# Optimization experiments

Hardware: AMD Instinct MI355X
Metric: run time of the kernel (lower is better)

## Reference

```python
import jax, jax.numpy as jnp
import numpy as np

FILTER_LENGTH = 800
HOP_LENGTH = 200
WIN_LENGTH = 800
NUM_SAMPLES = 8_000_000


def _make_forward_basis():
    # Real/imag DFT rows (cutoff = N/2+1) times a periodic Hamming window.
    fl, wl = FILTER_LENGTH, WIN_LENGTH
    fourier = np.fft.fft(np.eye(fl))
    cutoff = fl // 2 + 1  # 401
    basis = np.vstack([fourier[:cutoff].real, fourier[:cutoff].imag])  # [802, 800]
    n = np.arange(wl)
    window = 0.54 - 0.46 * np.cos(2.0 * np.pi * n / wl)  # scipy get_window('hamming', wl, fftbins=True)
    basis = basis * window[None, :]
    return jnp.asarray(basis[:, None, :], dtype=jnp.float32)  # [802, 1, 800] (OIH)


def setup_inputs() -> dict:
    key = jax.random.key(0)
    input_data = jax.random.normal(key, (NUM_SAMPLES,), dtype=jnp.float32)
    forward_basis = _make_forward_basis()
    return {"input_data": input_data, "forward_basis": forward_basis}


def reference(input_data, forward_basis):
    fl, hop = FILTER_LENGTH, HOP_LENGTH
    cutoff = fl // 2 + 1
    x = input_data.reshape(1, 1, -1)  # (N=1, C=1, T)
    x = jnp.pad(x, ((0, 0), (0, 0), (fl // 2, fl // 2)), mode='reflect')
    # Strided conv with the dense DFT basis == framed windowed DFT.
    out = jax.lax.conv_general_dilated(
        x, forward_basis, window_strides=(hop,), padding='VALID',
        dimension_numbers=('NCH', 'OIH', 'NCH'))  # [1, 802, n_frames]
    real = out[:, :cutoff, :]
    imag = out[:, cutoff:, :]
    magnitude = jnp.sqrt(real * real + imag * imag)  # [1, 401, n_frames]
    return magnitude
```

## Files before the change

kernel.cpp:

```cpp
#include <hip/hip_runtime.h>


#define FL   800
#define HOP  200
#define CUT  401
#define NS   8000000
#define NT   40001
#define KSTEPS 25

#define FT   64
#define TT   128
#define SLICE_SH 26624
#define XBN  8016000
#define BB_OFF 16032000

typedef short short8 __attribute__((ext_vector_type(8)));
typedef float float4v __attribute__((ext_vector_type(4)));

#define GU32 const __attribute__((address_space(1))) unsigned int*
#define LU32 __attribute__((address_space(3))) unsigned int*

__device__ inline unsigned short f2bf(float f) {
    union { float f; unsigned u; } v; v.f = f;
    unsigned r = v.u + 0x7FFFu + ((v.u >> 16) & 1u);
    return (unsigned short)(r >> 16);
}

__global__ void prep_x(const float* __restrict__ x, short* __restrict__ xb) {
    const int n8 = XBN / 8;
    for (int j = blockIdx.x * blockDim.x + threadIdx.x; j < n8;
         j += gridDim.x * blockDim.x) {
        const int i = j * 8;
        const int s = i - 400;
        short8 o;
        if (s >= 0 && s + 7 < NS) {
            const float4v a = *reinterpret_cast<const float4v*>(x + s);
            const float4v b = *reinterpret_cast<const float4v*>(x + s + 4);
            o[0]=f2bf(a[0]); o[1]=f2bf(a[1]); o[2]=f2bf(a[2]); o[3]=f2bf(a[3]);
            o[4]=f2bf(b[0]); o[5]=f2bf(b[1]); o[6]=f2bf(b[2]); o[7]=f2bf(b[3]);
        } else {
            #pragma unroll
            for (int q = 0; q < 8; ++q) {
                int sq = s + q;
                if (sq < 0) sq = -sq;
                else if (sq >= NS) sq = 2 * NS - 2 - sq;
                o[q] = f2bf(x[sq]);
            }
        }
        *reinterpret_cast<short8*>(xb + i) = o;
    }
}

__global__ void prep_b(const float* __restrict__ basis, short* __restrict__ bb) {
    const int nch = 896 * 100;
    for (int j = blockIdx.x * blockDim.x + threadIdx.x; j < nch;
         j += gridDim.x * blockDim.x) {
        const int row = j / 100;
        const int col = (j % 100) * 8;
        short8 o;
        int src = -1;
        if (row < CUT) src = row;
        else if (row >= 448 && row < 448 + CUT) src = row - 47;
        if (src >= 0) {
            const float* p = basis + (size_t)src * 800 + col;
            const float4v a = *reinterpret_cast<const float4v*>(p);
            const float4v b = *reinterpret_cast<const float4v*>(p + 4);
            o[0]=f2bf(a[0]); o[1]=f2bf(a[1]); o[2]=f2bf(a[2]); o[3]=f2bf(a[3]);
            o[4]=f2bf(b[0]); o[5]=f2bf(b[1]); o[6]=f2bf(b[2]); o[7]=f2bf(b[3]);
        } else {
            #pragma unroll
            for (int q = 0; q < 8; ++q) o[q] = 0;
        }
        *reinterpret_cast<short8*>(bb + (size_t)row * 800 + col) = o;
    }
}

#define MF(A, X, C) C = __builtin_amdgcn_mfma_f32_16x16x32_bf16((A), (X), (C), 0, 0, 0)

#define BODY(KS, BP, IKS, IBP, DOISS)                                           \
  {                                                                             \
    asm volatile("s_waitcnt vmcnt(2)" ::: "memory");                            \
    __builtin_amdgcn_s_barrier();                                               \
    asm volatile("" ::: "memory");                                              \
    const short* bp_ = (BP);                                                    \
    const short8 ar0 = *reinterpret_cast<const short8*>(bp_ + oar0);            \
    const short8 ar1 = *reinterpret_cast<const short8*>(bp_ + oar1);            \
    const short8 ai0 = *reinterpret_cast<const short8*>(bp_ + oai0);            \
    const short8 ai1 = *reinterpret_cast<const short8*>(bp_ + oai1);            \
    const short8 xf0 = *reinterpret_cast<const short8*>(&sX[xbase + 0*3200 + (KS)*32]); \
    const short8 xf1 = *reinterpret_cast<const short8*>(&sX[xbase + 1*3200 + (KS)*32]); \
    const short8 xf2 = *reinterpret_cast<const short8*>(&sX[xbase + 2*3200 + (KS)*32]); \
    const short8 xf3 = *reinterpret_cast<const short8*>(&sX[xbase + 3*3200 + (KS)*32]); \
    if (DOISS) {                                                                \
      __builtin_amdgcn_global_load_lds((GU32)(bsrc0 + (IKS)*32),                \
          (LU32)((IBP) + tid*8), 16, 0, 0);                                     \
      __builtin_amdgcn_global_load_lds((GU32)(bsrc1 + (IKS)*32),                \
          (LU32)((IBP) + 2048 + tid*8), 16, 0, 0);                              \
    }                                                                           \
    MF(ar0, xf0, acc_r[0][0]); MF(ar0, xf1, acc_r[0][1]);                       \
    MF(ar0, xf2, acc_r[0][2]); MF(ar0, xf3, acc_r[0][3]);                       \
    MF(ar1, xf0, acc_r[1][0]); MF(ar1, xf1, acc_r[1][1]);                       \
    MF(ar1, xf2, acc_r[1][2]); MF(ar1, xf3, acc_r[1][3]);                       \
    MF(ai0, xf0, acc_i[0][0]); MF(ai0, xf1, acc_i[0][1]);                       \
    MF(ai0, xf2, acc_i[0][2]); MF(ai0, xf3, acc_i[0][3]);                       \
    MF(ai1, xf0, acc_i[1][0]); MF(ai1, xf1, acc_i[1][1]);                       \
    MF(ai1, xf2, acc_i[1][2]); MF(ai1, xf3, acc_i[1][3]);                       \
  }

__global__ __launch_bounds__(256, 2)
void stft_mag_kernel(const short* __restrict__ xb,
                     const short* __restrict__ bb,
                     float* __restrict__ out) {
    __shared__ short sX[SLICE_SH];
    __shared__ short sB0[128 * 32];
    __shared__ short sB1[128 * 32];
    __shared__ short sB2[128 * 32];

    const int tid = threadIdx.x;
    const int t0  = blockIdx.x * TT;
    const int f0  = blockIdx.y * FT;

    const int rowc  = tid >> 2;
    const int slot0 = (tid & 3) ^ ((tid >> 3) & 3);
    const short* bsrc0 = bb + (size_t)(f0 + rowc) * 800 + slot0 * 8;
    const short* bsrc1 = bb + (size_t)(448 + f0 + rowc) * 800 + slot0 * 8;

    __builtin_amdgcn_global_load_lds((GU32)(bsrc0), (LU32)(sB0 + tid*8), 16, 0, 0);
    __builtin_amdgcn_global_load_lds((GU32)(bsrc1), (LU32)(sB0 + 2048 + tid*8), 16, 0, 0);
    {
        const short* src = xb + (size_t)t0 * HOP + tid * 8;
        short* dst = sX + tid * 8;
        #pragma unroll
        for (int it = 0; it < 13; ++it) {
            __builtin_amdgcn_global_load_lds((GU32)(src + it * 2048),
                                             (LU32)(dst + it * 2048), 16, 0, 0);
        }
    }
    __builtin_amdgcn_global_load_lds((GU32)(bsrc0 + 32), (LU32)(sB1 + tid*8), 16, 0, 0);
    __builtin_amdgcn_global_load_lds((GU32)(bsrc1 + 32), (LU32)(sB1 + 2048 + tid*8), 16, 0, 0);

    const int wid  = tid >> 6;
    const int lane = tid & 63;
    const int wm   = wid >> 1;
    const int wn   = wid & 1;
    const int l15  = lane & 15;
    const int l4   = lane >> 4;

    const int rr0 = wm * 32 + l15;
    const int rr1 = wm * 32 + 16 + l15;
    const int oar0 = (rr0 * 4 + (l4 ^ ((rr0 >> 1) & 3))) * 8;
    const int oar1 = (rr1 * 4 + (l4 ^ ((rr1 >> 1) & 3))) * 8;
    const int oai0 = ((64 + rr0) * 4 + (l4 ^ (((64 + rr0) >> 1) & 3))) * 8;
    const int oai1 = ((64 + rr1) * 4 + (l4 ^ (((64 + rr1) >> 1) & 3))) * 8;
    const int xbase = (wn * 64 + l15) * HOP + l4 * 8;

    float4v acc_r[2][4] = {};
    float4v acc_i[2][4] = {};

    for (int jj = 0; jj < 24; jj += 3) {
        BODY(jj,     sB0, jj + 2,                      sB2, 1);
        BODY(jj + 1, sB1, (jj + 3 <= 24 ? jj + 3 : 24), sB0, 1);
        BODY(jj + 2, sB2, (jj + 4 <= 24 ? jj + 4 : 24), sB1, 1);
    }
    BODY(24, sB0, 0, sB1, 0);

    #pragma unroll
    for (int mi = 0; mi < 2; ++mi) {
        #pragma unroll
        for (int r = 0; r < 4; ++r) {
            const int f = f0 + wm * 32 + mi * 16 + l4 * 4 + r;
            if (f >= CUT) continue;
            #pragma unroll
            for (int ni = 0; ni < 4; ++ni) {
                const int t = t0 + wn * 64 + ni * 16 + l15;
                if (t < NT) {
                    const float vr = (mi == 0 ? acc_r[0][ni][r] : acc_r[1][ni][r]);
                    const float vi = (mi == 0 ? acc_i[0][ni][r] : acc_i[1][ni][r]);
                    out[(size_t)f * NT + t] = sqrtf(vr * vr + vi * vi);
                }
            }
        }
    }
}

extern "C" void kernel_launch(void* const* d_in, const int* in_sizes, int n_in,
                              void* d_out, int out_size, void* d_ws, size_t ws_size,
                              hipStream_t stream) {
    const float* x     = (const float*)d_in[0];
    const float* basis = (const float*)d_in[1];
    float* out = (float*)d_out;

    short* xb = (short*)d_ws;
    short* bb = (short*)((char*)d_ws + BB_OFF);

    prep_x<<<2048, 256, 0, stream>>>(x, xb);
    prep_b<<<350, 256, 0, stream>>>(basis, bb);

    const int ttiles = (NT + TT - 1) / TT;
    const int ftiles = (CUT + FT - 1) / FT;
    dim3 grid(ttiles, ftiles);
    stft_mag_kernel<<<grid, 256, 0, stream>>>(xb, bb, out);
}
```

Measured before the change: 96.14 us.

## Double-buffer LDS fragments in registers, add MFMA priority, remap blocks across XCDs

The main GEMM loop now prefetches the next k-step's A/B fragments from LDS into a second register set while the current MFMAs run. Global-to-LDS issue is moved ahead of the wait, and the MFMA block is wrapped in s_setprio. The 2D grid is flattened to 1D with an XCD-aware remap, so the 7 frequency tiles of one time tile land on the same XCD and share the input slice in L2. This costs more VGPRs, which could threaten the 2-waves-per-SIMD occupancy target.

```diff
diff --git a/kernel.cpp b/kernel.cpp
--- a/kernel.cpp
+++ b/kernel.cpp
@@ -77,34 +77,40 @@
 
 #define MF(A, X, C) C = __builtin_amdgcn_mfma_f32_16x16x32_bf16((A), (X), (C), 0, 0, 0)
 
-#define BODY(KS, BP, IKS, IBP, DOISS)                                           \
+#define BODY(KS, FC, FN, NXTBUF, ISSBUF)                                        \
   {                                                                             \
-    asm volatile("s_waitcnt vmcnt(2)" ::: "memory");                            \
+    if ((KS) <= 22) {                                                           \
+      __builtin_amdgcn_global_load_lds((GU32)(bsrc0 + ((KS)+2)*32),             \
+          (LU32)((ISSBUF) + tid*8), 16, 0, 0);                                  \
+      __builtin_amdgcn_global_load_lds((GU32)(bsrc1 + ((KS)+2)*32),             \
+          (LU32)((ISSBUF) + 2048 + tid*8), 16, 0, 0);                           \
+      asm volatile("s_waitcnt vmcnt(2) lgkmcnt(0)" ::: "memory");               \
+    } else {                                                                    \
+      asm volatile("s_waitcnt vmcnt(0) lgkmcnt(0)" ::: "memory");               \
+    }                                                                           \
     __builtin_amdgcn_s_barrier();                                               \
     asm volatile("" ::: "memory");                                              \
-    const short* bp_ = (BP);                                                    \
-    const short8 ar0 = *reinterpret_cast<const short8*>(bp_ + oar0);            \
-    const short8 ar1 = *reinterpret_cast<const short8*>(bp_ + oar1);            \
-    const short8 ai0 = *reinterpret_cast<const short8*>(bp_ + oai0);            \
-    const short8 ai1 = *reinterpret_cast<const short8*>(bp_ + oai1);            \
-    const short8 xf0 = *reinterpret_cast<const short8*>(&sX[xbase + 0*3200 + (KS)*32]); \
-    const short8 xf1 = *reinterpret_cast<const short8*>(&sX[xbase + 1*3200 + (KS)*32]); \
-    const short8 xf2 = *reinterpret_cast<const short8*>(&sX[xbase + 2*3200 + (KS)*32]); \
-    const short8 xf3 = *reinterpret_cast<const short8*>(&sX[xbase + 3*3200 + (KS)*32]); \
-    if (DOISS) {                                                                \
-      __builtin_amdgcn_global_load_lds((GU32)(bsrc0 + (IKS)*32),                \
-          (LU32)((IBP) + tid*8), 16, 0, 0);                                     \
-      __builtin_amdgcn_global_load_lds((GU32)(bsrc1 + (IKS)*32),                \
-          (LU32)((IBP) + 2048 + tid*8), 16, 0, 0);                              \
+    {                                                                           \
+      const short* np_ = (NXTBUF);                                              \
+      FN[0] = *reinterpret_cast<const short8*>(np_ + oar0);                     \
+      FN[1] = *reinterpret_cast<const short8*>(np_ + oar1);                     \
+      FN[2] = *reinterpret_cast<const short8*>(np_ + oai0);                     \
+      FN[3] = *reinterpret_cast<const short8*>(np_ + oai1);                     \
+      FN[4] = *reinterpret_cast<const short8*>(&sX[xbase + 0*3200 + ((KS)+1)*32]); \
+      FN[5] = *reinterpret_cast<const short8*>(&sX[xbase + 1*3200 + ((KS)+1)*32]); \
+      FN[6] = *reinterpret_cast<const short8*>(&sX[xbase + 2*3200 + ((KS)+1)*32]); \
+      FN[7] = *reinterpret_cast<const short8*>(&sX[xbase + 3*3200 + ((KS)+1)*32]); \
     }                                                                           \
-    MF(ar0, xf0, acc_r[0][0]); MF(ar0, xf1, acc_r[0][1]);                       \
-    MF(ar0, xf2, acc_r[0][2]); MF(ar0, xf3, acc_r[0][3]);                       \
-    MF(ar1, xf0, acc_r[1][0]); MF(ar1, xf1, acc_r[1][1]);                       \
-    MF(ar1, xf2, acc_r[1][2]); MF(ar1, xf3, acc_r[1][3]);                       \
-    MF(ai0, xf0, acc_i[0][0]); MF(ai0, xf1, acc_i[0][1]);                       \
-    MF(ai0, xf2, acc_i[0][2]); MF(ai0, xf3, acc_i[0][3]);                       \
-    MF(ai1, xf0, acc_i[1][0]); MF(ai1, xf1, acc_i[1][1]);                       \
-    MF(ai1, xf2, acc_i[1][2]); MF(ai1, xf3, acc_i[1][3]);                       \
+    __builtin_amdgcn_s_setprio(1);                                              \
+    MF(FC[0], FC[4], acc_r[0][0]); MF(FC[0], FC[5], acc_r[0][1]);               \
+    MF(FC[0], FC[6], acc_r[0][2]); MF(FC[0], FC[7], acc_r[0][3]);               \
+    MF(FC[1], FC[4], acc_r[1][0]); MF(FC[1], FC[5], acc_r[1][1]);               \
+    MF(FC[1], FC[6], acc_r[1][2]); MF(FC[1], FC[7], acc_r[1][3]);               \
+    MF(FC[2], FC[4], acc_i[0][0]); MF(FC[2], FC[5], acc_i[0][1]);               \
+    MF(FC[2], FC[6], acc_i[0][2]); MF(FC[2], FC[7], acc_i[0][3]);               \
+    MF(FC[3], FC[4], acc_i[1][0]); MF(FC[3], FC[5], acc_i[1][1]);               \
+    MF(FC[3], FC[6], acc_i[1][2]); MF(FC[3], FC[7], acc_i[1][3]);               \
+    __builtin_amdgcn_s_setprio(0);                                              \
   }
 
 __global__ __launch_bounds__(256, 2)
@@ -117,8 +123,14 @@
     __shared__ short sB2[128 * 32];
 
     const int tid = threadIdx.x;
-    const int t0  = blockIdx.x * TT;
-    const int f0  = blockIdx.y * FT;
+
+    const int nwg = 313 * 7;
+    const int q = nwg >> 3, r = nwg & 7;
+    const int bid = blockIdx.x;
+    const int xcd = bid & 7, idx = bid >> 3;
+    const int wgid = (xcd < r ? xcd * (q + 1) : r * (q + 1) + (xcd - r) * q) + idx;
+    const int t0 = (wgid / 7) * TT;
+    const int f0 = (wgid % 7) * FT;
 
     const int rowc  = tid >> 2;
     const int slot0 = (tid & 3) ^ ((tid >> 3) & 3);
@@ -157,25 +169,53 @@
     float4v acc_r[2][4] = {};
     float4v acc_i[2][4] = {};
 
-    for (int jj = 0; jj < 24; jj += 3) {
-        BODY(jj,     sB0, jj + 2,                      sB2, 1);
-        BODY(jj + 1, sB1, (jj + 3 <= 24 ? jj + 3 : 24), sB0, 1);
-        BODY(jj + 2, sB2, (jj + 4 <= 24 ? jj + 4 : 24), sB1, 1);
-    }
-    BODY(24, sB0, 0, sB1, 0);
+    short8 FA[8], FB[8];
+
+    asm volatile("s_waitcnt vmcnt(2)" ::: "memory");
+    __builtin_amdgcn_s_barrier();
+    asm volatile("" ::: "memory");
+    FA[0] = *reinterpret_cast<const short8*>(sB0 + oar0);
+    FA[1] = *reinterpret_cast<const short8*>(sB0 + oar1);
+    FA[2] = *reinterpret_cast<const short8*>(sB0 + oai0);
+    FA[3] = *reinterpret_cast<const short8*>(sB0 + oai1);
+    FA[4] = *reinterpret_cast<const short8*>(&sX[xbase + 0*3200]);
+    FA[5] = *reinterpret_cast<const short8*>(&sX[xbase + 1*3200]);
+    FA[6] = *reinterpret_cast<const short8*>(&sX[xbase + 2*3200]);
+    FA[7] = *reinterpret_cast<const short8*>(&sX[xbase + 3*3200]);
+
+    #pragma unroll
+    for (int jj = 0; jj < 24; jj += 6) {
+        BODY(jj + 0, FA, FB, sB1, sB2);
+        BODY(jj + 1, FB, FA, sB2, sB0);
+        BODY(jj + 2, FA, FB, sB0, sB1);
+        BODY(jj + 3, FB, FA, sB1, sB2);
+        BODY(jj + 4, FA, FB, sB2, sB0);
+        BODY(jj + 5, FB, FA, sB0, sB1);
+    }
+
+    __builtin_amdgcn_s_setprio(1);
+    MF(FA[0], FA[4], acc_r[0][0]); MF(FA[0], FA[5], acc_r[0][1]);
+    MF(FA[0], FA[6], acc_r[0][2]); MF(FA[0], FA[7], acc_r[0][3]);
+    MF(FA[1], FA[4], acc_r[1][0]); MF(FA[1], FA[5], acc_r[1][1]);
+    MF(FA[1], FA[6], acc_r[1][2]); MF(FA[1], FA[7], acc_r[1][3]);
+    MF(FA[2], FA[4], acc_i[0][0]); MF(FA[2], FA[5], acc_i[0][1]);
+    MF(FA[2], FA[6], acc_i[0][2]); MF(FA[2], FA[7], acc_i[0][3]);
+    MF(FA[3], FA[4], acc_i[1][0]); MF(FA[3], FA[5], acc_i[1][1]);
+    MF(FA[3], FA[6], acc_i[1][2]); MF(FA[3], FA[7], acc_i[1][3]);
+    __builtin_amdgcn_s_setprio(0);
 
     #pragma unroll
     for (int mi = 0; mi < 2; ++mi) {
         #pragma unroll
-        for (int r = 0; r < 4; ++r) {
-            const int f = f0 + wm * 32 + mi * 16 + l4 * 4 + r;
+        for (int rr = 0; rr < 4; ++rr) {
+            const int f = f0 + wm * 32 + mi * 16 + l4 * 4 + rr;
             if (f >= CUT) continue;
             #pragma unroll
             for (int ni = 0; ni < 4; ++ni) {
                 const int t = t0 + wn * 64 + ni * 16 + l15;
                 if (t < NT) {
-                    const float vr = (mi == 0 ? acc_r[0][ni][r] : acc_r[1][ni][r]);
-                    const float vi = (mi == 0 ? acc_i[0][ni][r] : acc_i[1][ni][r]);
+                    const float vr = (mi == 0 ? acc_r[0][ni][rr] : acc_r[1][ni][rr]);
+                    const float vi = (mi == 0 ? acc_i[0][ni][rr] : acc_i[1][ni][rr]);
                     out[(size_t)f * NT + t] = sqrtf(vr * vr + vi * vi);
                 }
             }
@@ -196,8 +236,5 @@
     prep_x<<<2048, 256, 0, stream>>>(x, xb);
     prep_b<<<350, 256, 0, stream>>>(basis, bb);
 
-    const int ttiles = (NT + TT - 1) / TT;
-    const int ftiles = (CUT + FT - 1) / FT;
-    dim3 grid(ttiles, ftiles);
-    stft_mag_kernel<<<grid, 256, 0, stream>>>(xb, bb, out);
-}
+    stft_mag_kernel<<<313 * 7, 256, 0, stream>>>(xb, bb, out);
+}
```

After: 83.72 us. 1.15x faster.
